# Kernel optimization log

Hardware: AMD Instinct MI355X
Metric: run time of the kernel (lower is better)

## Reference

```python
import jax, jax.numpy as jnp
import numpy as np

B, T, C = 2048, 64, 384  # batch, seq (== block_size), n_embd
HEAD = 64


def setup_inputs() -> dict:
    key = jax.random.key(0)
    k1, k2, k3, k4 = jax.random.split(key, 4)
    x = jax.random.normal(k1, (B, T, C), dtype=jnp.float32)
    Wq = jax.random.normal(k2, (C, HEAD), dtype=jnp.float32) * (C ** -0.5)
    Wk = jax.random.normal(k3, (C, HEAD), dtype=jnp.float32) * (C ** -0.5)
    Wv = jax.random.normal(k4, (C, HEAD), dtype=jnp.float32) * (C ** -0.5)
    return {"x": x, "Wq": Wq, "Wk": Wk, "Wv": Wv}


def reference(x, Wq, Wk, Wv):
    Bx, Tx, Cx = x.shape
    q = jnp.einsum('btc,ch->bth', x, Wq)
    k = jnp.einsum('btc,ch->bth', x, Wk)
    v = jnp.einsum('btc,ch->bth', x, Wv)
    # NOTE: original code scales by n_embd**-0.5 (C), not head_size**-0.5
    wei = jnp.einsum('bth,bsh->bts', q, k) * (Cx ** -0.5)
    causal = jnp.tril(jnp.ones((Tx, Tx), dtype=bool))  # tril[:T,:T]
    wei = jnp.where(causal, wei, -jnp.inf)
    wei = jax.nn.softmax(wei, axis=-1)
    # dropout is identity in eval mode
    out = jnp.einsum('bts,bsh->bth', wei, v)
    return out
```

## Files before the change

### kernel.cpp

```cpp
#include <hip/hip_runtime.h>
#include <stdint.h>

typedef _Float16 f16;
typedef _Float16 f16x8 __attribute__((ext_vector_type(8)));
typedef _Float16 f16x4 __attribute__((ext_vector_type(4)));
typedef float floatx4 __attribute__((ext_vector_type(4)));
typedef float floatx2 __attribute__((ext_vector_type(2)));

#define TT 64
#define CDIM 384
#define HH 64
#define NKK 12
#define LDP 72
#define OST 66
#define CHUNK 12288
#define WBUF 6144
#define SCALE 0.05103103630798288f

__global__ void prep_w(const float* __restrict__ Wq,
                       const float* __restrict__ Wk,
                       const float* __restrict__ Wv,
                       f16* __restrict__ wf) {
    int t = blockIdx.x * 256 + threadIdx.x;
    if (t >= 3 * NKK * 4 * 64) return;
    int lane = t & 63;
    int tile = (t >> 6) & 3;
    int p    = (t >> 8) % 3;
    int kk   = t / 768;
    const float* W = (p == 0) ? Wq : ((p == 1) ? Wk : Wv);
    int n  = tile * 16 + (lane & 15);
    int k0 = kk * 32 + (lane >> 4) * 8;
    f16x8 frag;
#pragma unroll
    for (int j = 0; j < 8; ++j) frag[j] = (f16)W[(k0 + j) * HH + n];
    ((f16x8*)wf)[t] = frag;
}

static __device__ __forceinline__ f16x8 cvt8(float4 f0, float4 f1) {
    f16x8 h;
    h[0]=(f16)f0.x; h[1]=(f16)f0.y; h[2]=(f16)f0.z; h[3]=(f16)f0.w;
    h[4]=(f16)f1.x; h[5]=(f16)f1.y; h[6]=(f16)f1.z; h[7]=(f16)f1.w;
    return h;
}

static __device__ __forceinline__ void glds16(const void* g, void* l) {
    __builtin_amdgcn_global_load_lds(
        (const __attribute__((address_space(1))) uint32_t*)g,
        (__attribute__((address_space(3))) uint32_t*)l, 16, 0, 0);
}

__launch_bounds__(256, 4)
__global__ void attn_head(const float* __restrict__ x,
                          const f16* __restrict__ wf,
                          float* __restrict__ out) {
    __shared__ __align__(16) char smem[4 * TT * LDP * sizeof(f16)];
    f16* wbuf = (f16*)smem;
    f16* qs   = (f16*)smem;
    f16* ksm  = qs  + TT * LDP;
    f16* vst  = ksm + TT * LDP;
    f16* ps   = vst + TT * LDP;
    float* ost = (float*)smem;

    const int b    = blockIdx.x;
    const int tid  = threadIdx.x;
    const int wave = tid >> 6;
    const int lane = tid & 63;
    const int quad = lane >> 4;
    const int cl   = lane & 15;
    const int row0 = wave * 16;

    const floatx4 fzero = {0.f, 0.f, 0.f, 0.f};
    floatx4 acc[12];
#pragma unroll
    for (int T = 0; T < 12; ++T) acc[T] = fzero;

    const float* xp = x + ((size_t)b * TT + row0 + cl) * CDIM + quad * 8;
    const char* wb  = (const char*)wf;
    const int lslot = (wave * 64 + lane) * 16;

    float4 xa[3], xb[3];
#pragma unroll
    for (int j = 0; j < 3; ++j)
        glds16(wb + j * 4096 + lslot, wbuf + 0 * WBUF + j * 2048 + wave * 512);
    asm volatile("" ::: "memory");
    xa[0] = *(const float4*)(xp);
    xb[0] = *(const float4*)(xp + 4);
#pragma unroll
    for (int j = 0; j < 3; ++j)
        glds16(wb + CHUNK + j * 4096 + lslot, wbuf + 1 * WBUF + j * 2048 + wave * 512);
    xa[1] = *(const float4*)(xp + 32);
    xb[1] = *(const float4*)(xp + 36);

#pragma unroll
    for (int kk = 0; kk < NKK; ++kk) {
        if (kk < NKK - 1) asm volatile("s_waitcnt vmcnt(5)" ::: "memory");
        else              asm volatile("s_waitcnt vmcnt(0)" ::: "memory");
        __builtin_amdgcn_s_barrier();
        if (kk + 2 < NKK) {
            const int nb = (kk + 2) % 3;
#pragma unroll
            for (int j = 0; j < 3; ++j)
                glds16(wb + (kk + 2) * CHUNK + j * 4096 + lslot,
                       wbuf + nb * WBUF + j * 2048 + wave * 512);
            xa[nb] = *(const float4*)(xp + (kk + 2) * 32);
            xb[nb] = *(const float4*)(xp + (kk + 2) * 32 + 4);
        }
        f16x8 xf = cvt8(xa[kk % 3], xb[kk % 3]);
        const f16* wc = wbuf + (kk % 3) * WBUF;
        __builtin_amdgcn_s_setprio(1);
#pragma unroll
        for (int T = 0; T < 12; ++T) {
            f16x8 bf = *(const f16x8*)&wc[(T * 64 + lane) * 8];
            acc[T] = __builtin_amdgcn_mfma_f32_16x16x32_f16(xf, bf, acc[T], 0, 0, 0);
        }
        __builtin_amdgcn_s_setprio(0);
    }
    __syncthreads();

#pragma unroll
    for (int T = 0; T < 12; ++T) {
        int p = T >> 2;
        int h = (T & 3) * 16 + cl;
        if (p == 2) {
            f16x4 vv;
            vv[0]=(f16)acc[T][0]; vv[1]=(f16)acc[T][1];
            vv[2]=(f16)acc[T][2]; vv[3]=(f16)acc[T][3];
            *(f16x4*)&vst[h * LDP + row0 + quad * 4] = vv;
        } else if (p == 0) {
#pragma unroll
            for (int r = 0; r < 4; ++r)
                qs[(row0 + quad * 4 + r) * LDP + h] = (f16)(acc[T][r] * SCALE);
        } else {
#pragma unroll
            for (int r = 0; r < 4; ++r)
                ksm[(row0 + quad * 4 + r) * LDP + h] = (f16)acc[T][r];
        }
    }
    __syncthreads();

    floatx4 sa[4];
#pragma unroll
    for (int t = 0; t < 4; ++t) sa[t] = fzero;
#pragma unroll
    for (int kv = 0; kv < 2; ++kv) {
        f16x8 aq = *(const f16x8*)&qs[(row0 + cl) * LDP + kv * 32 + quad * 8];
#pragma unroll
        for (int t = 0; t < 4; ++t) {
            f16x8 bk = *(const f16x8*)&ksm[(t * 16 + cl) * LDP + kv * 32 + quad * 8];
            sa[t] = __builtin_amdgcn_mfma_f32_16x16x32_f16(aq, bk, sa[t], 0, 0, 0);
        }
    }

#pragma unroll
    for (int t = 0; t < 4; ++t) {
        int s = t * 16 + cl;
#pragma unroll
        for (int r = 0; r < 4; ++r) {
            int tr = row0 + quad * 4 + r;
            float p = (s <= tr) ? __expf(sa[t][r]) : 0.0f;
            ps[tr * LDP + s] = (f16)p;
        }
    }
    __syncthreads();

    floatx4 oa[4];
    floatx4 den = fzero;
#pragma unroll
    for (int t = 0; t < 4; ++t) oa[t] = fzero;
    f16x8 ones;
#pragma unroll
    for (int j = 0; j < 8; ++j) ones[j] = (f16)1.0f;
#pragma unroll
    for (int kv = 0; kv < 2; ++kv) {
        f16x8 ap = *(const f16x8*)&ps[(row0 + cl) * LDP + kv * 32 + quad * 8];
        den = __builtin_amdgcn_mfma_f32_16x16x32_f16(ap, ones, den, 0, 0, 0);
#pragma unroll
        for (int t = 0; t < 4; ++t) {
            f16x8 bv = *(const f16x8*)&vst[(t * 16 + cl) * LDP + kv * 32 + quad * 8];
            oa[t] = __builtin_amdgcn_mfma_f32_16x16x32_f16(ap, bv, oa[t], 0, 0, 0);
        }
    }
    float rden[4];
#pragma unroll
    for (int r = 0; r < 4; ++r) rden[r] = 1.0f / den[r];

#pragma unroll
    for (int t = 0; t < 4; ++t)
#pragma unroll
        for (int r = 0; r < 4; ++r)
            ost[(row0 + quad * 4 + r) * OST + t * 16 + cl] = oa[t][r] * rden[r];
    __syncthreads();

    float* op = out + (size_t)b * TT * HH;
#pragma unroll
    for (int i = 0; i < 4; ++i) {
        int row = i * 16 + (tid >> 4);
        int c4  = (tid & 15) * 4;
        floatx2 lo = *(const floatx2*)&ost[row * OST + c4];
        floatx2 hi = *(const floatx2*)&ost[row * OST + c4 + 2];
        float4 v; v.x = lo[0]; v.y = lo[1]; v.z = hi[0]; v.w = hi[1];
        *(float4*)&op[row * HH + c4] = v;
    }
}

extern "C" void kernel_launch(void* const* d_in, const int* in_sizes, int n_in,
                              void* d_out, int out_size, void* d_ws, size_t ws_size,
                              hipStream_t stream) {
    const float* x  = (const float*)d_in[0];
    const float* Wq = (const float*)d_in[1];
    const float* Wk = (const float*)d_in[2];
    const float* Wv = (const float*)d_in[3];
    float* out = (float*)d_out;
    f16* wf = (f16*)d_ws;

    prep_w<<<36, 256, 0, stream>>>(Wq, Wk, Wv, wf);
    attn_head<<<2048, 256, 0, stream>>>(x, wf, out);
}
```

Measured before the change: 299.9 us.

## Shrink LDS footprint to fit five blocks per CU with double-buffered weights

Cuts shared memory from four 64x72 f16 arenas to three by switching the weight-chunk staging from triple to double buffering and aliasing the P matrix onto the Q arena. Launch bounds rise from 4 to 5 blocks per CU so more blocks can be resident to hide latency. In exchange, prefetch distance drops to one chunk, so each chunk's load is less hidden, and two extra block-wide barriers are added to make the buffer aliasing safe.

After: 301.3 us. About the same (+0.5%).

```diff
diff --git a/kernel.cpp b/kernel.cpp
--- a/kernel.cpp
+++ b/kernel.cpp
@@ -14,7 +14,8 @@
 #define LDP 72
 #define OST 66
 #define CHUNK 12288
-#define WBUF 6144
+#define WBUFH 6144
+#define ARENA 4608
 #define SCALE 0.05103103630798288f
 
 __global__ void prep_w(const float* __restrict__ Wq,
@@ -49,16 +50,16 @@
         (__attribute__((address_space(3))) uint32_t*)l, 16, 0, 0);
 }
 
-__launch_bounds__(256, 4)
+__launch_bounds__(256, 5)
 __global__ void attn_head(const float* __restrict__ x,
                           const f16* __restrict__ wf,
                           float* __restrict__ out) {
-    __shared__ __align__(16) char smem[4 * TT * LDP * sizeof(f16)];
+    __shared__ __align__(16) char smem[3 * TT * LDP * sizeof(f16)];
     f16* wbuf = (f16*)smem;
     f16* qs   = (f16*)smem;
-    f16* ksm  = qs  + TT * LDP;
-    f16* vst  = ksm + TT * LDP;
-    f16* ps   = vst + TT * LDP;
+    f16* ksm  = qs + ARENA;
+    f16* vst  = qs + 2 * ARENA;
+    f16* ps   = qs;
     float* ost = (float*)smem;
 
     const int b    = blockIdx.x;
@@ -78,35 +79,33 @@
     const char* wb  = (const char*)wf;
     const int lslot = (wave * 64 + lane) * 16;
 
-    float4 xa[3], xb[3];
+    float4 xa[2], xb[2];
 #pragma unroll
     for (int j = 0; j < 3; ++j)
-        glds16(wb + j * 4096 + lslot, wbuf + 0 * WBUF + j * 2048 + wave * 512);
+        glds16(wb + j * 4096 + lslot, wbuf + j * 2048 + wave * 512);
     asm volatile("" ::: "memory");
     xa[0] = *(const float4*)(xp);
     xb[0] = *(const float4*)(xp + 4);
-#pragma unroll
-    for (int j = 0; j < 3; ++j)
-        glds16(wb + CHUNK + j * 4096 + lslot, wbuf + 1 * WBUF + j * 2048 + wave * 512);
-    xa[1] = *(const float4*)(xp + 32);
-    xb[1] = *(const float4*)(xp + 36);
+    asm volatile("" ::: "memory");
 
 #pragma unroll
     for (int kk = 0; kk < NKK; ++kk) {
-        if (kk < NKK - 1) asm volatile("s_waitcnt vmcnt(5)" ::: "memory");
-        else              asm volatile("s_waitcnt vmcnt(0)" ::: "memory");
+        if (kk == NKK - 1) asm volatile("s_waitcnt vmcnt(0)" ::: "memory");
+        else               asm volatile("s_waitcnt vmcnt(2)" ::: "memory");
         __builtin_amdgcn_s_barrier();
-        if (kk + 2 < NKK) {
-            const int nb = (kk + 2) % 3;
+        if (kk + 1 < NKK) {
+            const int nb = (kk + 1) & 1;
 #pragma unroll
             for (int j = 0; j < 3; ++j)
-                glds16(wb + (kk + 2) * CHUNK + j * 4096 + lslot,
-                       wbuf + nb * WBUF + j * 2048 + wave * 512);
-            xa[nb] = *(const float4*)(xp + (kk + 2) * 32);
-            xb[nb] = *(const float4*)(xp + (kk + 2) * 32 + 4);
-        }
-        f16x8 xf = cvt8(xa[kk % 3], xb[kk % 3]);
-        const f16* wc = wbuf + (kk % 3) * WBUF;
+                glds16(wb + (kk + 1) * CHUNK + j * 4096 + lslot,
+                       wbuf + nb * WBUFH + j * 2048 + wave * 512);
+            asm volatile("" ::: "memory");
+            xa[nb] = *(const float4*)(xp + (kk + 1) * 32);
+            xb[nb] = *(const float4*)(xp + (kk + 1) * 32 + 4);
+            asm volatile("" ::: "memory");
+        }
+        f16x8 xf = cvt8(xa[kk & 1], xb[kk & 1]);
+        const f16* wc = wbuf + (kk & 1) * WBUFH;
         __builtin_amdgcn_s_setprio(1);
 #pragma unroll
         for (int T = 0; T < 12; ++T) {
@@ -150,6 +149,7 @@
             sa[t] = __builtin_amdgcn_mfma_f32_16x16x32_f16(aq, bk, sa[t], 0, 0, 0);
         }
     }
+    __syncthreads();
 
 #pragma unroll
     for (int t = 0; t < 4; ++t) {
@@ -183,6 +183,7 @@
     float rden[4];
 #pragma unroll
     for (int r = 0; r < 4; ++r) rden[r] = 1.0f / den[r];
+    __syncthreads();
 
 #pragma unroll
     for (int t = 0; t < 4; ++t)
```
